# Kernel optimization log

Measured on AMD Instinct MI355X. Metric: run time of the kernel, lower is better.

## Reference

```python
import jax, jax.numpy as jnp
import numpy as np

NUM_CATEGORIES = 64
INPUT_DIM = 256
HIDDEN_DIM = 256
N = 4096  # number of samples (each with its own category)
M = 16    # rows per sample


def setup_inputs() -> dict:
    key = jax.random.key(0)
    k_x, k_cat, k_W = jax.random.split(key, 3)
    x = jax.random.normal(k_x, (N, M, INPUT_DIM), dtype=jnp.float32)
    cat_ids = jax.random.randint(k_cat, (N,), 0, NUM_CATEGORIES, dtype=jnp.int64)
    W = 0.02 * jax.random.normal(k_W, (NUM_CATEGORIES, INPUT_DIM, HIDDEN_DIM), dtype=jnp.float32)
    b = jnp.zeros((NUM_CATEGORIES, HIDDEN_DIM), dtype=jnp.float32)
    return {"x": x, "cat_ids": cat_ids, "W": W, "b": b}


def reference(x, cat_ids, W, b):
    # Gather per-sample weights/biases, then batched matmul + bias add.
    selected_W = W[cat_ids]              # [N, input_dim, hidden_dim]
    selected_b = b[cat_ids]              # [N, hidden_dim]
    out = jnp.einsum('nmi,nih->nmh', x, selected_W) + selected_b[:, None, :]
    return out
```

## Files before the change

kernel.cpp:

```cpp
#include <hip/hip_runtime.h>
#include <hip/hip_bf16.h>
#include <stdint.h>

#define N_SAMPLES 4096
#define M_ROWS 16
#define K_DIM 256
#define H_DIM 256
#define N_CATS 64
#define SPB 4
#define MAX_PADDED (N_SAMPLES + N_CATS * (SPB - 1))
#define NGROUP (MAX_PADDED / SPB)
#define GPX (NGROUP / 8)
#define GEMM_GRID (NGROUP * 2)
#define AROW_STRIDE 264

typedef _Float16 half8 __attribute__((ext_vector_type(8)));
typedef float floatx4 __attribute__((ext_vector_type(4)));

#define WT_BYTES ((size_t)N_CATS * K_DIM * H_DIM * 2)
#define ORD_OFF  WT_BYTES
#define WS_NEED  (ORD_OFF + (size_t)MAX_PADDED * 4)

__global__ __launch_bounds__(256)
void prep_combined(const float* __restrict__ W, _Float16* __restrict__ Wt,
                   const int* __restrict__ cat, int* __restrict__ ord) {
  const int tid = threadIdx.x;
  if (blockIdx.x < 1024) {
    __shared__ _Float16 t[64][72];
    const int bid = blockIdx.x;
    const int c  = bid >> 4;
    const int kb = (bid >> 2) & 3;
    const int hb = bid & 3;
    const int r  = tid >> 2;
    const int cg = (tid & 3) * 16;
    const float* src = W + ((size_t)c << 16) + (size_t)(kb * 64 + r) * 256 + hb * 64 + cg;
#pragma unroll
    for (int j = 0; j < 16; j += 4) {
      float4 v = *(const float4*)(src + j);
      t[r][cg + j + 0] = (_Float16)v.x;
      t[r][cg + j + 1] = (_Float16)v.y;
      t[r][cg + j + 2] = (_Float16)v.z;
      t[r][cg + j + 3] = (_Float16)v.w;
    }
    __syncthreads();
    _Float16* dst = Wt + ((size_t)c << 16) + (size_t)(hb * 64 + r) * 256 + kb * 64 + cg;
    half8 o0, o1;
#pragma unroll
    for (int j = 0; j < 8; j++) o0[j] = t[cg + j][r];
#pragma unroll
    for (int j = 0; j < 8; j++) o1[j] = t[cg + 8 + j][r];
    *(half8*)(dst) = o0;
    *(half8*)(dst + 8) = o1;
  } else {
    __shared__ int hist[N_CATS];
    __shared__ int poffs[N_CATS];
    __shared__ int curs[N_CATS];
    if (tid < N_CATS) hist[tid] = 0;
    for (int i = tid; i < MAX_PADDED; i += 256) ord[i] = -1;
    __syncthreads();
    for (int i = tid; i < N_SAMPLES; i += 256) atomicAdd(&hist[cat[i]], 1);
    __syncthreads();
    if (tid == 0) {
      int run = 0;
      for (int c = 0; c < N_CATS; c++) {
        poffs[c] = run;
        run += ((hist[c] + SPB - 1) / SPB) * SPB;
      }
    }
    if (tid < N_CATS) curs[tid] = 0;
    __syncthreads();
    for (int i = tid; i < N_SAMPLES; i += 256) {
      int c = cat[i];
      int p = poffs[c] + atomicAdd(&curs[c], 1);
      ord[p] = i;
    }
  }
}

__global__ __launch_bounds__(256, 4)
void gemm_kernel(const float* __restrict__ x, const int* __restrict__ cat_ids,
                 const float* __restrict__ bias, const _Float16* __restrict__ Wt,
                 const int* __restrict__ ord, float* __restrict__ out) {
  __shared__ _Float16 sA[64 * AROW_STRIDE];
  __shared__ int s_meta[SPB];

  const int tid = threadIdx.x;
  const int B = blockIdx.x;
  const int xcd = B & 7;
  const int slot = B >> 3;
  const int h_half = slot & 1;
  const int group = xcd * GPX + (slot >> 1);
  const int h0 = h_half << 7;

  if (tid < SPB) s_meta[tid] = ord[group * SPB + tid];
  __syncthreads();
  const int s0 = s_meta[0];
  if (s0 < 0) return;
  const int cat = cat_ids[s0];

  const int wid  = tid >> 6;
  const int lane = tid & 63;
  const int l15  = lane & 15;
  const int quad = lane >> 4;

  const int r = tid >> 2;
  const int q = tid & 3;
  const int smp = s_meta[r >> 4];
  const float* asrc = (smp >= 0)
      ? (x + ((size_t)smp * 16 + (r & 15)) * K_DIM + q * 64) : nullptr;
  _Float16* adst = &sA[r * AROW_STRIDE];

#pragma unroll
  for (int hf = 0; hf < 2; hf++) {
    float4 v[8];
    if (asrc) {
#pragma unroll
      for (int j = 0; j < 8; j++) v[j] = ((const float4*)asrc)[hf * 8 + j];
    } else {
#pragma unroll
      for (int j = 0; j < 8; j++) v[j] = make_float4(0.f, 0.f, 0.f, 0.f);
    }
#pragma unroll
    for (int oj = 0; oj < 4; oj++) {
      half8 h;
      h[0] = (_Float16)v[oj * 2].x;     h[1] = (_Float16)v[oj * 2].y;
      h[2] = (_Float16)v[oj * 2].z;     h[3] = (_Float16)v[oj * 2].w;
      h[4] = (_Float16)v[oj * 2 + 1].x; h[5] = (_Float16)v[oj * 2 + 1].y;
      h[6] = (_Float16)v[oj * 2 + 1].z; h[7] = (_Float16)v[oj * 2 + 1].w;
      *(half8*)&adst[(q * 8 + hf * 4 + oj) * 8] = h;
    }
  }

  const _Float16* wbase = Wt + ((size_t)cat << 16);
  half8 bf[8][2];
#pragma unroll
  for (int kt = 0; kt < 8; kt++)
#pragma unroll
    for (int nt = 0; nt < 2; nt++) {
      const int col = h0 + wid * 32 + nt * 16 + l15;
      bf[kt][nt] = *(const half8*)(wbase + (size_t)col * K_DIM + kt * 32 + quad * 8);
    }

  floatx4 acc[4][2];
#pragma unroll
  for (int i = 0; i < 4; i++)
#pragma unroll
    for (int j = 0; j < 2; j++)
#pragma unroll
      for (int e = 0; e < 4; e++) acc[i][j][e] = 0.0f;

  __syncthreads();

#pragma unroll
  for (int kt = 0; kt < 8; kt++) {
    half8 af[4];
#pragma unroll
    for (int mt = 0; mt < 4; mt++)
      af[mt] = *(const half8*)&sA[(mt * 16 + l15) * AROW_STRIDE + (kt * 4 + quad) * 8];
#pragma unroll
    for (int mt = 0; mt < 4; mt++)
#pragma unroll
      for (int nt = 0; nt < 2; nt++)
        acc[mt][nt] = __builtin_amdgcn_mfma_f32_16x16x32_f16(af[mt], bf[kt][nt], acc[mt][nt], 0, 0, 0);
  }

  float bv[2];
#pragma unroll
  for (int nt = 0; nt < 2; nt++)
    bv[nt] = bias[cat * H_DIM + h0 + wid * 32 + nt * 16 + l15];
#pragma unroll
  for (int mt = 0; mt < 4; mt++) {
    int s = s_meta[mt];
    if (s < 0) continue;
    float* obase = out + (size_t)s * 16 * H_DIM;
#pragma unroll
    for (int nt = 0; nt < 2; nt++) {
      int col = h0 + wid * 32 + nt * 16 + l15;
#pragma unroll
      for (int rr = 0; rr < 4; rr++) {
        int row = quad * 4 + rr;
        obase[(size_t)row * H_DIM + col] = acc[mt][nt][rr] + bv[nt];
      }
    }
  }
}

__global__ __launch_bounds__(256)
void naive_kernel(const float* __restrict__ x, const int* __restrict__ cat,
                  const float* __restrict__ W, const float* __restrict__ bias,
                  float* __restrict__ out) {
  __shared__ float sx[16 * 256];
  const int n = blockIdx.x;
  const int tid = threadIdx.x;
  const int c = cat[n];
  const float* xs = x + (size_t)n * 16 * 256;
  for (int i = tid; i < 16 * 256; i += 256) sx[i] = xs[i];
  __syncthreads();
  const float* Wc = W + ((size_t)c << 16);
  float accv[16];
  float bv = bias[c * 256 + tid];
#pragma unroll
  for (int m = 0; m < 16; m++) accv[m] = bv;
  for (int k = 0; k < 256; k++) {
    float w = Wc[(size_t)k * 256 + tid];
#pragma unroll
    for (int m = 0; m < 16; m++) accv[m] += sx[m * 256 + k] * w;
  }
#pragma unroll
  for (int m = 0; m < 16; m++) out[((size_t)n * 16 + m) * 256 + tid] = accv[m];
}

extern "C" void kernel_launch(void* const* d_in, const int* in_sizes, int n_in,
                              void* d_out, int out_size, void* d_ws, size_t ws_size,
                              hipStream_t stream) {
  const float* x    = (const float*)d_in[0];
  const int*   cat  = (const int*)d_in[1];
  const float* W    = (const float*)d_in[2];
  const float* bias = (const float*)d_in[3];
  float* out = (float*)d_out;

  if (ws_size < WS_NEED) {
    naive_kernel<<<N_SAMPLES, 256, 0, stream>>>(x, cat, W, bias, out);
    return;
  }

  char* ws = (char*)d_ws;
  _Float16* Wt = (_Float16*)ws;
  int* ord = (int*)(ws + ORD_OFF);

  prep_combined<<<1025, 256, 0, stream>>>(W, Wt, cat, ord);
  gemm_kernel<<<GEMM_GRID, 256, 0, stream>>>(x, cat, bias, Wt, ord, out);
}
```

Before: 169.5 us.

## Precompute per-group category and split B-fragment loads to overlap with A staging

The prep kernel now writes a per-group category table, so the GEMM kernel reads its category and four sample ids with one vector load instead of an LDS round-trip, a barrier and a dependent cat_ids lookup. Half of the weight fragments are issued before the A tile is staged, and the other half are loaded inside the MFMA loop. The A staging is reorganised so each wave loads one sample's 16 rows with coalesced float4 reads. This shortens the kernel prologue dependency chain and overlaps weight loads with compute, at the cost of a slightly larger prep step and a different register schedule.

```diff
diff --git a/kernel.cpp b/kernel.cpp
--- a/kernel.cpp
+++ b/kernel.cpp
@@ -12,18 +12,21 @@
 #define NGROUP (MAX_PADDED / SPB)
 #define GPX (NGROUP / 8)
 #define GEMM_GRID (NGROUP * 2)
-#define AROW_STRIDE 264
+#define AROW 264
 
 typedef _Float16 half8 __attribute__((ext_vector_type(8)));
+typedef _Float16 half4 __attribute__((ext_vector_type(4)));
 typedef float floatx4 __attribute__((ext_vector_type(4)));
 
 #define WT_BYTES ((size_t)N_CATS * K_DIM * H_DIM * 2)
-#define ORD_OFF  WT_BYTES
+#define GCAT_OFF WT_BYTES
+#define ORD_OFF  (WT_BYTES + 4288)
 #define WS_NEED  (ORD_OFF + (size_t)MAX_PADDED * 4)
 
 __global__ __launch_bounds__(256)
 void prep_combined(const float* __restrict__ W, _Float16* __restrict__ Wt,
-                   const int* __restrict__ cat, int* __restrict__ ord) {
+                   const int* __restrict__ cat, int* __restrict__ ord,
+                   int* __restrict__ gcat) {
   const int tid = threadIdx.x;
   if (blockIdx.x < 1024) {
     __shared__ _Float16 t[64][72];
@@ -57,6 +60,7 @@
     __shared__ int curs[N_CATS];
     if (tid < N_CATS) hist[tid] = 0;
     for (int i = tid; i < MAX_PADDED; i += 256) ord[i] = -1;
+    for (int i = tid; i < NGROUP; i += 256) gcat[i] = 0;
     __syncthreads();
     for (int i = tid; i < N_SAMPLES; i += 256) atomicAdd(&hist[cat[i]], 1);
     __syncthreads();
@@ -69,6 +73,12 @@
     }
     if (tid < N_CATS) curs[tid] = 0;
     __syncthreads();
+    if (tid < N_CATS) {
+      const int c = tid;
+      const int g0 = poffs[c] >> 2;
+      const int ng = (hist[c] + SPB - 1) >> 2;
+      for (int g = 0; g < ng; g++) gcat[g0 + g] = c;
+    }
     for (int i = tid; i < N_SAMPLES; i += 256) {
       int c = cat[i];
       int p = poffs[c] + atomicAdd(&curs[c], 1);
@@ -78,11 +88,10 @@
 }
 
 __global__ __launch_bounds__(256, 4)
-void gemm_kernel(const float* __restrict__ x, const int* __restrict__ cat_ids,
-                 const float* __restrict__ bias, const _Float16* __restrict__ Wt,
-                 const int* __restrict__ ord, float* __restrict__ out) {
-  __shared__ _Float16 sA[64 * AROW_STRIDE];
-  __shared__ int s_meta[SPB];
+void gemm_kernel(const float* __restrict__ x, const float* __restrict__ bias,
+                 const _Float16* __restrict__ Wt, const int* __restrict__ ord,
+                 const int* __restrict__ gcat, float* __restrict__ out) {
+  __shared__ __align__(16) _Float16 sA[64 * AROW];
 
   const int tid = threadIdx.x;
   const int B = blockIdx.x;
@@ -92,54 +101,47 @@
   const int group = xcd * GPX + (slot >> 1);
   const int h0 = h_half << 7;
 
-  if (tid < SPB) s_meta[tid] = ord[group * SPB + tid];
-  __syncthreads();
-  const int s0 = s_meta[0];
-  if (s0 < 0) return;
-  const int cat = cat_ids[s0];
+  const int cat = gcat[group];
+  const int4 sm = *(const int4*)(ord + group * 4);
+  if (sm.x < 0) return;
 
   const int wid  = tid >> 6;
   const int lane = tid & 63;
   const int l15  = lane & 15;
   const int quad = lane >> 4;
 
-  const int r = tid >> 2;
-  const int q = tid & 3;
-  const int smp = s_meta[r >> 4];
-  const float* asrc = (smp >= 0)
-      ? (x + ((size_t)smp * 16 + (r & 15)) * K_DIM + q * 64) : nullptr;
-  _Float16* adst = &sA[r * AROW_STRIDE];
-
-#pragma unroll
-  for (int hf = 0; hf < 2; hf++) {
-    float4 v[8];
-    if (asrc) {
-#pragma unroll
-      for (int j = 0; j < 8; j++) v[j] = ((const float4*)asrc)[hf * 8 + j];
-    } else {
-#pragma unroll
-      for (int j = 0; j < 8; j++) v[j] = make_float4(0.f, 0.f, 0.f, 0.f);
-    }
-#pragma unroll
-    for (int oj = 0; oj < 4; oj++) {
-      half8 h;
-      h[0] = (_Float16)v[oj * 2].x;     h[1] = (_Float16)v[oj * 2].y;
-      h[2] = (_Float16)v[oj * 2].z;     h[3] = (_Float16)v[oj * 2].w;
-      h[4] = (_Float16)v[oj * 2 + 1].x; h[5] = (_Float16)v[oj * 2 + 1].y;
-      h[6] = (_Float16)v[oj * 2 + 1].z; h[7] = (_Float16)v[oj * 2 + 1].w;
-      *(half8*)&adst[(q * 8 + hf * 4 + oj) * 8] = h;
-    }
-  }
-
   const _Float16* wbase = Wt + ((size_t)cat << 16);
+
   half8 bf[8][2];
 #pragma unroll
-  for (int kt = 0; kt < 8; kt++)
+  for (int kt = 0; kt < 4; kt++)
 #pragma unroll
     for (int nt = 0; nt < 2; nt++) {
       const int col = h0 + wid * 32 + nt * 16 + l15;
       bf[kt][nt] = *(const half8*)(wbase + (size_t)col * K_DIM + kt * 32 + quad * 8);
     }
+  __builtin_amdgcn_sched_barrier(0);
+
+  const int smp = (wid == 0) ? sm.x : (wid == 1) ? sm.y : (wid == 2) ? sm.z : sm.w;
+  const float* asrc = (smp >= 0) ? (x + ((size_t)smp << 12)) : nullptr;
+  _Float16* adst = sA + (size_t)(wid * 16) * AROW;
+  if (asrc) {
+#pragma unroll
+    for (int j = 0; j < 16; j++) {
+      float4 v = *(const float4*)(asrc + j * 256 + lane * 4);
+      half4 h;
+      h[0] = (_Float16)v.x; h[1] = (_Float16)v.y;
+      h[2] = (_Float16)v.z; h[3] = (_Float16)v.w;
+      *(half4*)(adst + (size_t)j * AROW + lane * 4) = h;
+    }
+  } else {
+    half4 h;
+#pragma unroll
+    for (int e = 0; e < 4; e++) h[e] = (_Float16)0.0f;
+#pragma unroll
+    for (int j = 0; j < 16; j++)
+      *(half4*)(adst + (size_t)j * AROW + lane * 4) = h;
+  }
 
   floatx4 acc[4][2];
 #pragma unroll
@@ -153,10 +155,17 @@
 
 #pragma unroll
   for (int kt = 0; kt < 8; kt++) {
+    if (kt < 4) {
+#pragma unroll
+      for (int nt = 0; nt < 2; nt++) {
+        const int col = h0 + wid * 32 + nt * 16 + l15;
+        bf[kt + 4][nt] = *(const half8*)(wbase + (size_t)col * K_DIM + (kt + 4) * 32 + quad * 8);
+      }
+    }
     half8 af[4];
 #pragma unroll
     for (int mt = 0; mt < 4; mt++)
-      af[mt] = *(const half8*)&sA[(mt * 16 + l15) * AROW_STRIDE + (kt * 4 + quad) * 8];
+      af[mt] = *(const half8*)&sA[(size_t)(mt * 16 + l15) * AROW + kt * 32 + quad * 8];
 #pragma unroll
     for (int mt = 0; mt < 4; mt++)
 #pragma unroll
@@ -168,17 +177,18 @@
 #pragma unroll
   for (int nt = 0; nt < 2; nt++)
     bv[nt] = bias[cat * H_DIM + h0 + wid * 32 + nt * 16 + l15];
+  const int srow[4] = {sm.x, sm.y, sm.z, sm.w};
 #pragma unroll
   for (int mt = 0; mt < 4; mt++) {
-    int s = s_meta[mt];
+    const int s = srow[mt];
     if (s < 0) continue;
-    float* obase = out + (size_t)s * 16 * H_DIM;
+    float* obase = out + ((size_t)s << 12);
 #pragma unroll
     for (int nt = 0; nt < 2; nt++) {
-      int col = h0 + wid * 32 + nt * 16 + l15;
+      const int col = h0 + wid * 32 + nt * 16 + l15;
 #pragma unroll
       for (int rr = 0; rr < 4; rr++) {
-        int row = quad * 4 + rr;
+        const int row = quad * 4 + rr;
         obase[(size_t)row * H_DIM + col] = acc[mt][nt][rr] + bv[nt];
       }
     }
@@ -226,8 +236,9 @@
 
   char* ws = (char*)d_ws;
   _Float16* Wt = (_Float16*)ws;
-  int* ord = (int*)(ws + ORD_OFF);
-
-  prep_combined<<<1025, 256, 0, stream>>>(W, Wt, cat, ord);
-  gemm_kernel<<<GEMM_GRID, 256, 0, stream>>>(x, cat, bias, Wt, ord, out);
-}
+  int* gcat = (int*)(ws + GCAT_OFF);
+  int* ord  = (int*)(ws + ORD_OFF);
+
+  prep_combined<<<1025, 256, 0, stream>>>(W, Wt, cat, ord, gcat);
+  gemm_kernel<<<GEMM_GRID, 256, 0, stream>>>(x, bias, Wt, ord, gcat, out);
+}
```

New measurement: 161.2 us. 1.05x faster.
